# Kernel tuning notes

Measured on AMD Instinct MI355X. Metric: run time of the kernel, lower is better.

The kernel has to match this reference:

```python
import jax, jax.numpy as jnp
import numpy as np

N = 128
BATCH = 4096


def _legs_transition(n):
    # HiPPO-LegS transition matrices (measure='legs' branch of transition())
    q = np.arange(n, dtype=np.float64)
    col, row = np.meshgrid(q, q)
    r = 2 * q + 1
    M = -(np.where(row >= col, r, 0) - np.diag(q))
    T = np.sqrt(np.diag(2 * q + 1))
    A = T @ M @ np.linalg.inv(T)   # lower triangular
    B = np.diag(T)                 # (n,)
    return A.astype(np.float32), B.astype(np.float32)


def setup_inputs() -> dict:
    key = jax.random.key(0)
    k1, k2, k3 = jax.random.split(key, 3)
    A, B_vec = _legs_transition(N)
    u = jax.random.normal(k1, (BATCH, N), dtype=jnp.float32)
    v = jax.random.normal(k2, (BATCH,), dtype=jnp.float32)
    # per-example step sizes, realistic small dt
    delta = 0.001 + 0.01 * jax.random.uniform(k3, (BATCH,), dtype=jnp.float32)
    return {"u": u, "v": v, "delta": delta, "A": jnp.asarray(A), "B_vec": jnp.asarray(B_vec)}


def reference(u, v, delta, A, B_vec):
    """Bilinear (Tustin) update, alpha=0.5:
       x = (I - dt/2 A)^{-1} [ (I + dt/2 A) u + dt B v ]
    Matches ManualAdaptiveTransition.bilinear with tensor delta.
    """
    n = A.shape[0]
    dt2 = 0.5 * delta                                   # (B,)
    # forward_mult: (I + dt/2 A) u  == u + dt/2 * (A u)
    x = u + dt2[:, None] * jnp.einsum('ij,bj->bi', A, u)
    # add dt * B * v
    x = x + (delta * v)[:, None] * B_vec
    # inverse_mult: batched lower-triangular solve (I - dt/2 A) y = x
    mat = jnp.eye(n, dtype=u.dtype) - dt2[:, None, None] * A   # (B, n, n)
    solve = jax.vmap(lambda m, b: jax.scipy.linalg.solve_triangular(m, b, lower=True))
    x = solve(mat, x)
    return x
```

## Files before the change

### kernel.cpp

```cpp
#include <hip/hip_runtime.h>


#define HN 128

__global__ __launch_bounds__(256) void hippo_bilinear_wave_kernel(
    const float* __restrict__ u,
    const float* __restrict__ v,
    const float* __restrict__ delta,
    const float* __restrict__ Bv,
    float* __restrict__ out)
{
    const int lane = threadIdx.x & 63;
    const int row  = blockIdx.x * (blockDim.x >> 6) + (threadIdx.x >> 6);

    const float dlt = delta[row];
    const float dt2 = 0.5f * dlt;
    const float dv  = dlt * v[row];

    const float2 u2 = ((const float2*)(u + (size_t)row * HN))[lane];
    const float2 b2 = ((const float2*)Bv)[lane];

    const float u0 = u2.x, u1 = u2.y;
    const float v0 = b2.x, v1 = b2.y;
    const float ip1_0 = (float)(2 * lane + 1);
    const float ip1_1 = (float)(2 * lane + 2);

    const float p0 = v0 * u0;
    const float p1 = v1 * u1;
    const float ps = p0 + p1;
    float run = ps;
    #pragma unroll
    for (int d = 1; d < 64; d <<= 1) {
        const float t = __shfl_up(run, d, 64);
        if (lane >= d) run += t;
    }
    const float Pexcl = run - ps;
    const float P0 = Pexcl;
    const float P1 = Pexcl + p0;

    float x0 = fmaf(dt2, fmaf(-ip1_0, u0, -v0 * P0), u0);
    x0 = fmaf(dv, v0, x0);
    float x1 = fmaf(dt2, fmaf(-ip1_1, u1, -v1 * P1), u1);
    x1 = fmaf(dv, v1, x1);

    const float den0 = fmaf(dt2, ip1_0, 1.0f);
    const float den1 = fmaf(dt2, ip1_1, 1.0f);
    float r0 = __builtin_amdgcn_rcpf(den0);
    r0 = r0 * fmaf(-den0, r0, 2.0f);
    float r1 = __builtin_amdgcn_rcpf(den1);
    r1 = r1 * fmaf(-den1, r1, 2.0f);

    const float w0 = dt2 * v0;
    const float w1 = dt2 * v1;
    const float c0 = v0 * r0;
    const float c1 = v1 * r1;
    const float a0 = fmaf(-w0, c0, 1.0f);
    const float b0 = c0 * x0;
    const float a1 = fmaf(-w1, c1, 1.0f);
    const float b1 = c1 * x1;

    float Ai = a1 * a0;
    float Bi = fmaf(a1, b0, b1);

    #pragma unroll
    for (int d = 1; d < 64; d <<= 1) {
        const float tA = __shfl_up(Ai, d, 64);
        const float tB = __shfl_up(Bi, d, 64);
        if (lane >= d) {
            Bi = fmaf(Ai, tB, Bi);
            Ai = Ai * tA;
        }
    }
    const float Bprev = __shfl_up(Bi, 1, 64);
    const float Sin = (lane == 0) ? 0.0f : Bprev;

    const float y0 = fmaf(-w0, Sin, x0) * r0;
    const float S1 = fmaf(v0, y0, Sin);
    const float y1 = fmaf(-w1, S1, x1) * r1;

    float2 y2; y2.x = y0; y2.y = y1;
    ((float2*)(out + (size_t)row * HN))[lane] = y2;
}

extern "C" void kernel_launch(void* const* d_in, const int* in_sizes, int n_in,
                              void* d_out, int out_size, void* d_ws, size_t ws_size,
                              hipStream_t stream) {
    const float* u     = (const float*)d_in[0];
    const float* v     = (const float*)d_in[1];
    const float* delta = (const float*)d_in[2];
    const float* Bv    = (const float*)d_in[4];
    float* out = (float*)d_out;

    const int batch = in_sizes[1];
    const int rows_per_block = 4;
    hippo_bilinear_wave_kernel<<<dim3(batch / rows_per_block), dim3(256), 0, stream>>>(
        u, v, delta, Bv, out);
}
```

Measured before the change: 9.701 us.

## Fuse prefix-sum and linear-recurrence scans into a single wave scan

Replaces the two sequential wavefront scans (a prefix sum of B*u, then an affine recurrence scan) with one scan that carries four state values (p, a, q, k). The composed operator folds the P-dependent term into the recurrence, so the second scan no longer waits on the first. This halves the number of serial scan stages but doubles the shuffles per stage (four instead of one plus two), so shuffle count is roughly unchanged while latency depth drops.

```diff
diff --git a/kernel.cpp b/kernel.cpp
--- a/kernel.cpp
+++ b/kernel.cpp
@@ -3,7 +3,7 @@
 
 #define HN 128
 
-__global__ __launch_bounds__(256) void hippo_bilinear_wave_kernel(
+__global__ __launch_bounds__(256) void hippo_bilinear_fused_kernel(
     const float* __restrict__ u,
     const float* __restrict__ v,
     const float* __restrict__ delta,
@@ -22,61 +22,55 @@
 
     const float u0 = u2.x, u1 = u2.y;
     const float v0 = b2.x, v1 = b2.y;
-    const float ip1_0 = (float)(2 * lane + 1);
-    const float ip1_1 = (float)(2 * lane + 2);
+    const float ip0 = (float)(2 * lane + 1);
+    const float ip1 = (float)(2 * lane + 2);
 
-    const float p0 = v0 * u0;
-    const float p1 = v1 * u1;
-    const float ps = p0 + p1;
-    float run = ps;
-    #pragma unroll
-    for (int d = 1; d < 64; d <<= 1) {
-        const float t = __shfl_up(run, d, 64);
-        if (lane >= d) run += t;
-    }
-    const float Pexcl = run - ps;
-    const float P0 = Pexcl;
-    const float P1 = Pexcl + p0;
+    const float den0 = fmaf(dt2, ip0, 1.0f);
+    const float den1 = fmaf(dt2, ip1, 1.0f);
+    float r0 = __builtin_amdgcn_rcpf(den0); r0 = r0 * fmaf(-den0, r0, 2.0f);
+    float r1 = __builtin_amdgcn_rcpf(den1); r1 = r1 * fmaf(-den1, r1, 2.0f);
 
-    float x0 = fmaf(dt2, fmaf(-ip1_0, u0, -v0 * P0), u0);
-    x0 = fmaf(dv, v0, x0);
-    float x1 = fmaf(dt2, fmaf(-ip1_1, u1, -v1 * P1), u1);
-    x1 = fmaf(dv, v1, x1);
+    const float w0 = dt2 * v0, w1 = dt2 * v1;
+    const float c0 = v0 * r0,  c1 = v1 * r1;
 
-    const float den0 = fmaf(dt2, ip1_0, 1.0f);
-    const float den1 = fmaf(dt2, ip1_1, 1.0f);
-    float r0 = __builtin_amdgcn_rcpf(den0);
-    r0 = r0 * fmaf(-den0, r0, 2.0f);
-    float r1 = __builtin_amdgcn_rcpf(den1);
-    r1 = r1 * fmaf(-den1, r1, 2.0f);
+    float g0 = fmaf(-dt2 * ip0, u0, u0); g0 = fmaf(dv, v0, g0);
+    float g1 = fmaf(-dt2 * ip1, u1, u1); g1 = fmaf(dv, v1, g1);
 
-    const float w0 = dt2 * v0;
-    const float w1 = dt2 * v1;
-    const float c0 = v0 * r0;
-    const float c1 = v1 * r1;
-    const float a0 = fmaf(-w0, c0, 1.0f);
-    const float b0 = c0 * x0;
-    const float a1 = fmaf(-w1, c1, 1.0f);
-    const float b1 = c1 * x1;
+    const float p0 = v0 * u0, p1 = v1 * u1;
+    const float a0 = fmaf(-w0, c0, 1.0f), a1 = fmaf(-w1, c1, 1.0f);
+    const float q0 = a0 - 1.0f, q1 = a1 - 1.0f;
+    const float k0 = c0 * g0,   k1 = c1 * g1;
 
-    float Ai = a1 * a0;
-    float Bi = fmaf(a1, b0, b1);
+    float pL = p0 + p1;
+    float kL = fmaf(q1, p0, fmaf(a1, k0, k1));
+    float qL = fmaf(a1, q0, q1);
+    float aL = a1 * a0;
 
     #pragma unroll
     for (int d = 1; d < 64; d <<= 1) {
-        const float tA = __shfl_up(Ai, d, 64);
-        const float tB = __shfl_up(Bi, d, 64);
+        const float tp = __shfl_up(pL, d, 64);
+        const float ta = __shfl_up(aL, d, 64);
+        const float tq = __shfl_up(qL, d, 64);
+        const float tk = __shfl_up(kL, d, 64);
         if (lane >= d) {
-            Bi = fmaf(Ai, tB, Bi);
-            Ai = Ai * tA;
+            kL = fmaf(qL, tp, fmaf(aL, tk, kL));
+            qL = fmaf(aL, tq, qL);
+            aL *= ta;
+            pL += tp;
         }
     }
-    const float Bprev = __shfl_up(Bi, 1, 64);
-    const float Sin = (lane == 0) ? 0.0f : Bprev;
 
+    const float Pprev = __shfl_up(pL, 1, 64);
+    const float Sprev = __shfl_up(kL, 1, 64);
+    const float Pin = (lane == 0) ? 0.0f : Pprev;
+    const float Sin = (lane == 0) ? 0.0f : Sprev;
+
+    const float x0 = fmaf(-w0, Pin, g0);
     const float y0 = fmaf(-w0, Sin, x0) * r0;
-    const float S1 = fmaf(v0, y0, Sin);
-    const float y1 = fmaf(-w1, S1, x1) * r1;
+    const float Pm = fmaf(v0, u0, Pin);
+    const float Sm = fmaf(v0, y0, Sin);
+    const float x1 = fmaf(-w1, Pm, g1);
+    const float y1 = fmaf(-w1, Sm, x1) * r1;
 
     float2 y2; y2.x = y0; y2.y = y1;
     ((float2*)(out + (size_t)row * HN))[lane] = y2;
@@ -92,7 +86,6 @@
     float* out = (float*)d_out;
 
     const int batch = in_sizes[1];
-    const int rows_per_block = 4;
-    hippo_bilinear_wave_kernel<<<dim3(batch / rows_per_block), dim3(256), 0, stream>>>(
+    hippo_bilinear_fused_kernel<<<dim3(batch / 4), dim3(256), 0, stream>>>(
         u, v, delta, Bv, out);
 }
```

New measurement: 9.506 us. -2.0%, faster.
